# Optimization experiments

Hardware: AMD Instinct MI355X
Metric: run time of the kernel (lower is better)

Reference implementation:

```python
import jax, jax.numpy as jnp
import numpy as np

# Model/config constants
N = 2048          # total nodes in batch
G = 32            # number of graphs
NPG = 64          # nodes per graph (N = G * NPG)
E = 16384         # total edges (E//G per graph, unique within graph)
HIDDEN = 256
N_HEADS = 8
HEAD_DIM = HIDDEN // N_HEADS
EDGE_FEAT = 16
SCALE = HEAD_DIM ** -0.5


def setup_inputs() -> dict:
    key = jax.random.key(0)
    ks = jax.random.split(key, 16)
    nodes = jax.random.normal(ks[0], (N, HIDDEN), dtype=jnp.float32)
    edges = jax.random.normal(ks[1], (E, EDGE_FEAT), dtype=jnp.float32)
    n_node = jnp.full((G,), NPG, dtype=jnp.int32)
    # Unique (sender, receiver) pairs within each graph block
    epg = E // G
    gkeys = jax.random.split(ks[2], G)
    perm = jax.vmap(lambda k: jax.random.permutation(k, NPG * NPG)[:epg])(gkeys)  # [G, epg]
    so = perm // NPG
    ro = perm % NPG
    base = (jnp.arange(G, dtype=jnp.int32) * NPG)[:, None]
    senders = (base + so).reshape(-1).astype(jnp.int32)
    receivers = (base + ro).reshape(-1).astype(jnp.int32)
    init = 0.02
    Wq = jax.random.normal(ks[3], (HIDDEN, HIDDEN), jnp.float32) * init
    Wk = jax.random.normal(ks[4], (HIDDEN, HIDDEN), jnp.float32) * init
    Wv = jax.random.normal(ks[5], (HIDDEN, HIDDEN), jnp.float32) * init
    Wo = jax.random.normal(ks[6], (HIDDEN, HIDDEN), jnp.float32) * init
    We = jax.random.normal(ks[7], (EDGE_FEAT, N_HEADS), jnp.float32) * init
    bq = jnp.zeros((HIDDEN,), jnp.float32)
    bk = jnp.zeros((HIDDEN,), jnp.float32)
    bv = jnp.zeros((HIDDEN,), jnp.float32)
    bo = jnp.zeros((HIDDEN,), jnp.float32)
    be = jnp.zeros((N_HEADS,), jnp.float32)
    return {"nodes": nodes, "edges": edges, "n_node": n_node,
            "senders": senders, "receivers": receivers,
            "Wq": Wq, "bq": bq, "Wk": Wk, "bk": bk, "Wv": Wv, "bv": bv,
            "Wo": Wo, "bo": bo, "We": We, "be": be}


def reference(nodes, edges, n_node, senders, receivers,
              Wq, bq, Wk, bk, Wv, bv, Wo, bo, We, be):
    n_nodes = nodes.shape[0]
    n_graphs = n_node.shape[0]
    q = (nodes @ Wq + bq).reshape(n_nodes, N_HEADS, HEAD_DIM)
    k = (nodes @ Wk + bk).reshape(n_nodes, N_HEADS, HEAD_DIM)
    v = (nodes @ Wv + bv).reshape(n_nodes, N_HEADS, HEAD_DIM)
    scores = jnp.einsum('ihd,jhd->ijh', q, k) * SCALE  # [N, N, H]
    graph_idx = jnp.repeat(jnp.arange(n_graphs), n_node, total_repeat_length=n_nodes)
    same_graph = graph_idx[:, None] == graph_idx[None, :]
    scores = scores + jnp.where(same_graph[:, :, None], 0.0, -1e9)
    # Edge bias scattered into [N, N, H] at (receiver, sender)
    edge_bias = edges @ We + be  # [E, H]
    edge_bias_matrix = jnp.zeros((n_nodes, n_nodes, N_HEADS), dtype=scores.dtype)
    edge_bias_matrix = edge_bias_matrix.at[receivers, senders].set(edge_bias)
    scores = scores + edge_bias_matrix
    attn = jax.nn.softmax(scores, axis=1)  # softmax over key axis j
    out = jnp.einsum('ijh,jhd->ihd', attn, v).reshape(n_nodes, HIDDEN)
    return out @ Wo + bo
```

## Files before the change

### kernel.cpp

```cpp
#include <hip/hip_runtime.h>

#define N_NODES 2048
#define N_GRAPHS 32
#define NPG 64
#define N_EDGES 16384
#define EPG 512
#define HIDDEN 256
#define NHEADS 8
#define HEADDIM 32
#define EDGEFEAT 16
#define ATT_SCALE 0.17677669529663687f

typedef unsigned short u16;
typedef __attribute__((ext_vector_type(8))) short bf16x8;
typedef __attribute__((ext_vector_type(4))) float f32x4;

__device__ __forceinline__ u16 f2b(float f) {
    unsigned x = __float_as_uint(f);
    return (u16)((x + 0x7fffu + ((x >> 16) & 1u)) >> 16);
}
__device__ __forceinline__ unsigned pack2(float a, float b) {
    return (unsigned)f2b(a) | ((unsigned)f2b(b) << 16);
}

__global__ __launch_bounds__(256)
void prep_kernel(const float* __restrict__ Wq, const float* __restrict__ Wk,
                 const float* __restrict__ Wv, const float* __restrict__ Wo,
                 const float* __restrict__ edges, const float* __restrict__ We,
                 const float* __restrict__ be,
                 u16* __restrict__ WT, float* __restrict__ ebias)
{
    const int b = blockIdx.x, tid = threadIdx.x;
    __shared__ float shm[64 * 65];

    if (b < 64) {
        if (tid < EDGEFEAT * NHEADS) shm[tid] = We[tid];
        if (tid < NHEADS) shm[128 + tid] = be[tid];
        __syncthreads();
        const int e = b * 256 + tid;
        const float* ef = edges + (size_t)e * EDGEFEAT;
        float f[EDGEFEAT];
        *(float4*)&f[0]  = *(const float4*)(ef + 0);
        *(float4*)&f[4]  = *(const float4*)(ef + 4);
        *(float4*)&f[8]  = *(const float4*)(ef + 8);
        *(float4*)&f[12] = *(const float4*)(ef + 12);
        float a[NHEADS];
        #pragma unroll
        for (int h = 0; h < NHEADS; ++h) a[h] = shm[128 + h];
        #pragma unroll
        for (int i = 0; i < EDGEFEAT; ++i)
            #pragma unroll
            for (int h = 0; h < NHEADS; ++h) a[h] += f[i] * shm[i * 8 + h];
        float* dst = ebias + (size_t)e * NHEADS;
        *(float4*)(dst)     = make_float4(a[0], a[1], a[2], a[3]);
        *(float4*)(dst + 4) = make_float4(a[4], a[5], a[6], a[7]);
    } else {
        const int bb = b - 64;
        const int m = bb >> 4, t = bb & 15;
        const int k0 = (t >> 2) * 64, n0 = (t & 3) * 64;
        const float* src = (m == 0) ? Wq : (m == 1) ? Wk : (m == 2) ? Wv : Wo;
        #pragma unroll
        for (int rep = 0; rep < 4; ++rep) {
            const int q = rep * 256 + tid;
            const int row = q >> 4, c4 = (q & 15) * 4;
            float4 x = *(const float4*)(src + (size_t)(k0 + row) * HIDDEN + n0 + c4);
            shm[row * 65 + c4 + 0] = x.x;
            shm[row * 65 + c4 + 1] = x.y;
            shm[row * 65 + c4 + 2] = x.z;
            shm[row * 65 + c4 + 3] = x.w;
        }
        __syncthreads();
        u16* dst = WT + (size_t)m * HIDDEN * HIDDEN;
        #pragma unroll
        for (int rep = 0; rep < 2; ++rep) {
            const int nl = (tid >> 3) + rep * 32;
            const int k8 = (tid & 7) * 8;
            uint4 o;
            o.x = pack2(shm[(k8 + 0) * 65 + nl], shm[(k8 + 1) * 65 + nl]);
            o.y = pack2(shm[(k8 + 2) * 65 + nl], shm[(k8 + 3) * 65 + nl]);
            o.z = pack2(shm[(k8 + 4) * 65 + nl], shm[(k8 + 5) * 65 + nl]);
            o.w = pack2(shm[(k8 + 6) * 65 + nl], shm[(k8 + 7) * 65 + nl]);
            *(uint4*)(dst + (size_t)(n0 + nl) * HIDDEN + k0 + k8) = o;
        }
    }
}

__global__ __launch_bounds__(256)
void qkv_attn_kernel(const float* __restrict__ nodes,
                     const u16* __restrict__ WT,
                     const float* __restrict__ bq, const float* __restrict__ bk,
                     const float* __restrict__ bv,
                     const float* __restrict__ ebias,
                     const int* __restrict__ senders,
                     const int* __restrict__ receivers,
                     u16* __restrict__ attnb)
{
    const int g = blockIdx.x, h = blockIdx.y;
    const int tid = threadIdx.x;
    const int lane = tid & 63, wv = tid >> 6;
    const int l16 = lane & 15, quad = lane >> 4;

    __shared__ __align__(16) unsigned char smem[84480];
    short* An = (short*)smem;
    short* Wt = (short*)smem + 64 * 264;
    float* qs = (float*)smem;
    float* ks = qs + 64 * 33;
    float* vs = ks + 64 * 33;
    float* sc = vs + 64 * 33;
    float* red = sc + 64 * 65;

    #pragma unroll
    for (int rep = 0; rep < 16; ++rep) {
        const int q = rep * 256 + tid;
        const int row = q >> 6, f4 = q & 63;
        float4 x = *(const float4*)(nodes + (size_t)(g * NPG + row) * HIDDEN + f4 * 4);
        *(uint2*)&An[row * 264 + f4 * 4] = make_uint2(pack2(x.x, x.y), pack2(x.z, x.w));
    }
    #pragma unroll
    for (int m = 0; m < 3; ++m) {
        const u16* src = WT + (size_t)m * HIDDEN * HIDDEN + (size_t)(h * HEADDIM) * HIDDEN;
        #pragma unroll
        for (int rep = 0; rep < 4; ++rep) {
            const int q = rep * 256 + tid;
            const int row = q >> 5, u = q & 31;
            uint4 x = *(const uint4*)(src + (size_t)row * HIDDEN + u * 8);
            *(uint4*)&Wt[(m * 32 + row) * 264 + u * 8] = x;
        }
    }
    __syncthreads();

    f32x4 acc[6];
    #pragma unroll
    for (int nt = 0; nt < 6; ++nt) acc[nt] = (f32x4){0.f, 0.f, 0.f, 0.f};
    const int arow = (wv * 16 + l16) * 264 + quad * 8;
    #pragma unroll
    for (int k0 = 0; k0 < HIDDEN; k0 += 32) {
        bf16x8 af = *(const bf16x8*)&An[arow + k0];
        #pragma unroll
        for (int nt = 0; nt < 6; ++nt) {
            bf16x8 bf = *(const bf16x8*)&Wt[(nt * 16 + l16) * 264 + k0 + quad * 8];
            acc[nt] = __builtin_amdgcn_mfma_f32_16x16x32_bf16(af, bf, acc[nt], 0, 0, 0);
        }
    }
    __syncthreads();

    #pragma unroll
    for (int nt = 0; nt < 6; ++nt) {
        const int tns = nt >> 1;
        const int col = (nt & 1) * 16 + l16;
        const float* bp = (tns == 0) ? bq : (tns == 1) ? bk : bv;
        const float bias = bp[h * HEADDIM + col];
        float* dst = (tns == 0) ? qs : (tns == 1) ? ks : vs;
        #pragma unroll
        for (int r = 0; r < 4; ++r)
            dst[(wv * 16 + quad * 4 + r) * 33 + col] = acc[nt][r] + bias;
    }
    __syncthreads();

    const int i  = tid & 63;
    const int cg = tid >> 6;

    {
        float qr[HEADDIM];
        #pragma unroll
        for (int d = 0; d < HEADDIM; ++d) qr[d] = qs[i * 33 + d];
        #pragma unroll
        for (int jj = 0; jj < 16; ++jj) {
            const int j = cg * 16 + jj;
            float s = 0.f;
            #pragma unroll
            for (int d = 0; d < HEADDIM; ++d) s += qr[d] * ks[j * 33 + d];
            sc[i * 65 + j] = s * ATT_SCALE;
        }
    }
    __syncthreads();

    {
        #pragma unroll
        for (int rep = 0; rep < 2; ++rep) {
            const int e = g * EPG + rep * 256 + tid;
            const float b = ebias[(size_t)e * NHEADS + h];
            const int s_l = senders[e] & (NPG - 1);
            const int r_l = receivers[e] & (NPG - 1);
            sc[r_l * 65 + s_l] += b;
        }
    }
    __syncthreads();

    {
        float* red_m = red;
        float* red_s = red + 4 * 64;
        float m = -1e30f;
        #pragma unroll
        for (int jj = 0; jj < 16; ++jj) m = fmaxf(m, sc[i * 65 + cg * 16 + jj]);
        red_m[cg * 64 + i] = m;
        __syncthreads();
        m = fmaxf(fmaxf(red_m[0 * 64 + i], red_m[1 * 64 + i]),
                  fmaxf(red_m[2 * 64 + i], red_m[3 * 64 + i]));
        float s = 0.f;
        #pragma unroll
        for (int jj = 0; jj < 16; ++jj) {
            const int j = cg * 16 + jj;
            float e = __expf(sc[i * 65 + j] - m);
            sc[i * 65 + j] = e;
            s += e;
        }
        red_s[cg * 64 + i] = s;
        __syncthreads();
        const float inv = 1.f / (red_s[0 * 64 + i] + red_s[1 * 64 + i] +
                                 red_s[2 * 64 + i] + red_s[3 * 64 + i]);
        #pragma unroll
        for (int jj = 0; jj < 16; ++jj) sc[i * 65 + cg * 16 + jj] *= inv;
    }
    __syncthreads();

    {
        const int row = tid >> 2;
        const int d0 = (tid & 3) * 8;
        float a8[8] = {0, 0, 0, 0, 0, 0, 0, 0};
        for (int j = 0; j < NPG; ++j) {
            const float p = sc[row * 65 + j];
            #pragma unroll
            for (int dd = 0; dd < 8; ++dd) a8[dd] += p * vs[j * 33 + d0 + dd];
        }
        uint4 o;
        o.x = pack2(a8[0], a8[1]);
        o.y = pack2(a8[2], a8[3]);
        o.z = pack2(a8[4], a8[5]);
        o.w = pack2(a8[6], a8[7]);
        *(uint4*)(attnb + (size_t)(g * NPG + row) * HIDDEN + h * HEADDIM + d0) = o;
    }
}

__global__ __launch_bounds__(256)
void outproj_kernel(const u16* __restrict__ A,
                    const u16* __restrict__ BT,
                    const float* __restrict__ bo,
                    float* __restrict__ C)
{
    const int n0 = blockIdx.x * 64, m0 = blockIdx.y * 64;
    const int tid = threadIdx.x;
    const int lane = tid & 63, wv = tid >> 6;
    const int l16 = lane & 15, quad = lane >> 4;

    __shared__ __align__(16) short Ab[64 * 264];
    __shared__ __align__(16) short Bb[64 * 264];

    #pragma unroll
    for (int rep = 0; rep < 8; ++rep) {
        const int q = rep * 256 + tid;
        const int row = q >> 5, u = q & 31;
        *(uint4*)&Ab[row * 264 + u * 8] = *(const uint4*)(A + (size_t)(m0 + row) * HIDDEN + u * 8);
        *(uint4*)&Bb[row * 264 + u * 8] = *(const uint4*)(BT + (size_t)(n0 + row) * HIDDEN + u * 8);
    }
    __syncthreads();

    f32x4 acc[4];
    #pragma unroll
    for (int nt = 0; nt < 4; ++nt) acc[nt] = (f32x4){0.f, 0.f, 0.f, 0.f};
    const int arow = (wv * 16 + l16) * 264 + quad * 8;
    #pragma unroll
    for (int k0 = 0; k0 < HIDDEN; k0 += 32) {
        bf16x8 af = *(const bf16x8*)&Ab[arow + k0];
        #pragma unroll
        for (int nt = 0; nt < 4; ++nt) {
            bf16x8 bf = *(const bf16x8*)&Bb[(nt * 16 + l16) * 264 + k0 + quad * 8];
            acc[nt] = __builtin_amdgcn_mfma_f32_16x16x32_bf16(af, bf, acc[nt], 0, 0, 0);
        }
    }

    #pragma unroll
    for (int nt = 0; nt < 4; ++nt) {
        const int col = n0 + nt * 16 + l16;
        const float bias = bo[col];
        #pragma unroll
        for (int r = 0; r < 4; ++r)
            C[(size_t)(m0 + wv * 16 + quad * 4 + r) * HIDDEN + col] = acc[nt][r] + bias;
    }
}

extern "C" void kernel_launch(void* const* d_in, const int* in_sizes, int n_in,
                              void* d_out, int out_size, void* d_ws, size_t ws_size,
                              hipStream_t stream)
{
    const float* nodes     = (const float*)d_in[0];
    const float* edges     = (const float*)d_in[1];
    const int*   senders   = (const int*)d_in[3];
    const int*   receivers = (const int*)d_in[4];
    const float* Wq = (const float*)d_in[5];
    const float* bq = (const float*)d_in[6];
    const float* Wk = (const float*)d_in[7];
    const float* bk = (const float*)d_in[8];
    const float* Wv = (const float*)d_in[9];
    const float* bv = (const float*)d_in[10];
    const float* Wo = (const float*)d_in[11];
    const float* bo = (const float*)d_in[12];
    const float* We = (const float*)d_in[13];
    const float* be = (const float*)d_in[14];
    float* out = (float*)d_out;

    u16*   WT    = (u16*)d_ws;
    float* ebias = (float*)(WT + (size_t)4 * HIDDEN * HIDDEN);
    u16*   attnb = (u16*)(ebias + (size_t)N_EDGES * NHEADS);
    u16*   WoT   = WT + (size_t)3 * HIDDEN * HIDDEN;

    prep_kernel<<<dim3(128), dim3(256), 0, stream>>>(Wq, Wk, Wv, Wo, edges, We, be,
                                                     WT, ebias);
    qkv_attn_kernel<<<dim3(N_GRAPHS, NHEADS), dim3(256), 0, stream>>>(
        nodes, WT, bq, bk, bv, ebias, senders, receivers, attnb);
    outproj_kernel<<<dim3(HIDDEN / 64, N_NODES / 64), dim3(256), 0, stream>>>(
        attnb, WoT, bo, out);
}
```

Before: 99.47 us.

## Fuse weight prep and edge bias into attention kernels, use MFMA for scores

Drops the separate prep kernel. Weight transpose and bf16 conversion now happen inside the attention and output-projection kernels, and the edge bias is computed per head inline. QK^T and PV are moved from scalar FP32 loops to bf16 MFMA, with a hi/lo split to keep accuracy close to FP32. This removes one launch and a workspace round trip. In exchange, each block redoes the weight conversion, the transposing shared-memory stores are strided and may bank-conflict, and the split-precision approach adds extra MFMAs.

Result: faster. 93.70 us, median of 2 (-5.8%).

```diff
diff --git a/kernel.cpp b/kernel.cpp
--- a/kernel.cpp
+++ b/kernel.cpp
@@ -19,81 +19,23 @@
     unsigned x = __float_as_uint(f);
     return (u16)((x + 0x7fffu + ((x >> 16) & 1u)) >> 16);
 }
+__device__ __forceinline__ float b2f(u16 u) {
+    return __uint_as_float(((unsigned)u) << 16);
+}
 __device__ __forceinline__ unsigned pack2(float a, float b) {
     return (unsigned)f2b(a) | ((unsigned)f2b(b) << 16);
 }
 
 __global__ __launch_bounds__(256)
-void prep_kernel(const float* __restrict__ Wq, const float* __restrict__ Wk,
-                 const float* __restrict__ Wv, const float* __restrict__ Wo,
-                 const float* __restrict__ edges, const float* __restrict__ We,
-                 const float* __restrict__ be,
-                 u16* __restrict__ WT, float* __restrict__ ebias)
-{
-    const int b = blockIdx.x, tid = threadIdx.x;
-    __shared__ float shm[64 * 65];
-
-    if (b < 64) {
-        if (tid < EDGEFEAT * NHEADS) shm[tid] = We[tid];
-        if (tid < NHEADS) shm[128 + tid] = be[tid];
-        __syncthreads();
-        const int e = b * 256 + tid;
-        const float* ef = edges + (size_t)e * EDGEFEAT;
-        float f[EDGEFEAT];
-        *(float4*)&f[0]  = *(const float4*)(ef + 0);
-        *(float4*)&f[4]  = *(const float4*)(ef + 4);
-        *(float4*)&f[8]  = *(const float4*)(ef + 8);
-        *(float4*)&f[12] = *(const float4*)(ef + 12);
-        float a[NHEADS];
-        #pragma unroll
-        for (int h = 0; h < NHEADS; ++h) a[h] = shm[128 + h];
-        #pragma unroll
-        for (int i = 0; i < EDGEFEAT; ++i)
-            #pragma unroll
-            for (int h = 0; h < NHEADS; ++h) a[h] += f[i] * shm[i * 8 + h];
-        float* dst = ebias + (size_t)e * NHEADS;
-        *(float4*)(dst)     = make_float4(a[0], a[1], a[2], a[3]);
-        *(float4*)(dst + 4) = make_float4(a[4], a[5], a[6], a[7]);
-    } else {
-        const int bb = b - 64;
-        const int m = bb >> 4, t = bb & 15;
-        const int k0 = (t >> 2) * 64, n0 = (t & 3) * 64;
-        const float* src = (m == 0) ? Wq : (m == 1) ? Wk : (m == 2) ? Wv : Wo;
-        #pragma unroll
-        for (int rep = 0; rep < 4; ++rep) {
-            const int q = rep * 256 + tid;
-            const int row = q >> 4, c4 = (q & 15) * 4;
-            float4 x = *(const float4*)(src + (size_t)(k0 + row) * HIDDEN + n0 + c4);
-            shm[row * 65 + c4 + 0] = x.x;
-            shm[row * 65 + c4 + 1] = x.y;
-            shm[row * 65 + c4 + 2] = x.z;
-            shm[row * 65 + c4 + 3] = x.w;
-        }
-        __syncthreads();
-        u16* dst = WT + (size_t)m * HIDDEN * HIDDEN;
-        #pragma unroll
-        for (int rep = 0; rep < 2; ++rep) {
-            const int nl = (tid >> 3) + rep * 32;
-            const int k8 = (tid & 7) * 8;
-            uint4 o;
-            o.x = pack2(shm[(k8 + 0) * 65 + nl], shm[(k8 + 1) * 65 + nl]);
-            o.y = pack2(shm[(k8 + 2) * 65 + nl], shm[(k8 + 3) * 65 + nl]);
-            o.z = pack2(shm[(k8 + 4) * 65 + nl], shm[(k8 + 5) * 65 + nl]);
-            o.w = pack2(shm[(k8 + 6) * 65 + nl], shm[(k8 + 7) * 65 + nl]);
-            *(uint4*)(dst + (size_t)(n0 + nl) * HIDDEN + k0 + k8) = o;
-        }
-    }
-}
-
-__global__ __launch_bounds__(256)
-void qkv_attn_kernel(const float* __restrict__ nodes,
-                     const u16* __restrict__ WT,
-                     const float* __restrict__ bq, const float* __restrict__ bk,
-                     const float* __restrict__ bv,
-                     const float* __restrict__ ebias,
-                     const int* __restrict__ senders,
-                     const int* __restrict__ receivers,
-                     u16* __restrict__ attnb)
+void qkv_attn_fused(const float* __restrict__ nodes,
+                    const float* __restrict__ Wq, const float* __restrict__ Wk,
+                    const float* __restrict__ Wv,
+                    const float* __restrict__ bq, const float* __restrict__ bk,
+                    const float* __restrict__ bv,
+                    const float* __restrict__ edges, const float* __restrict__ We,
+                    const float* __restrict__ be,
+                    const int* __restrict__ senders, const int* __restrict__ receivers,
+                    u16* __restrict__ attnb)
 {
     const int g = blockIdx.x, h = blockIdx.y;
     const int tid = threadIdx.x;
@@ -103,11 +45,18 @@
     __shared__ __align__(16) unsigned char smem[84480];
     short* An = (short*)smem;
     short* Wt = (short*)smem + 64 * 264;
-    float* qs = (float*)smem;
-    float* ks = qs + 64 * 33;
-    float* vs = ks + 64 * 33;
-    float* sc = vs + 64 * 33;
+    short* qhi = (short*)smem;
+    short* qlo = qhi + 64 * 40;
+    short* khi = qlo + 64 * 40;
+    short* klo = khi + 64 * 40;
+    short* vsT = klo + 64 * 40;
+    float* sc  = (float*)(smem + 25088);
     float* red = sc + 64 * 65;
+    __shared__ float we_h[EDGEFEAT];
+    __shared__ float sbe;
+
+    if (tid < EDGEFEAT) we_h[tid] = We[tid * NHEADS + h];
+    if (tid == 0) sbe = be[h];
 
     #pragma unroll
     for (int rep = 0; rep < 16; ++rep) {
@@ -117,15 +66,17 @@
         *(uint2*)&An[row * 264 + f4 * 4] = make_uint2(pack2(x.x, x.y), pack2(x.z, x.w));
     }
     #pragma unroll
-    for (int m = 0; m < 3; ++m) {
-        const u16* src = WT + (size_t)m * HIDDEN * HIDDEN + (size_t)(h * HEADDIM) * HIDDEN;
-        #pragma unroll
-        for (int rep = 0; rep < 4; ++rep) {
-            const int q = rep * 256 + tid;
-            const int row = q >> 5, u = q & 31;
-            uint4 x = *(const uint4*)(src + (size_t)row * HIDDEN + u * 8);
-            *(uint4*)&Wt[(m * 32 + row) * 264 + u * 8] = x;
-        }
+    for (int rep = 0; rep < 24; ++rep) {
+        const int q = rep * 256 + tid;
+        const float* Wp = (rep < 8) ? Wq : (rep < 16) ? Wk : Wv;
+        const int r = q & 2047;
+        const int krow = r >> 3, f4 = r & 7;
+        float4 x = *(const float4*)(Wp + (size_t)krow * HIDDEN + h * HEADDIM + f4 * 4);
+        const int nb = (rep >> 3) * 32 + f4 * 4;
+        Wt[(nb + 0) * 264 + krow] = (short)f2b(x.x);
+        Wt[(nb + 1) * 264 + krow] = (short)f2b(x.y);
+        Wt[(nb + 2) * 264 + krow] = (short)f2b(x.z);
+        Wt[(nb + 3) * 264 + krow] = (short)f2b(x.w);
     }
     __syncthreads();
 
@@ -150,44 +101,62 @@
         const int col = (nt & 1) * 16 + l16;
         const float* bp = (tns == 0) ? bq : (tns == 1) ? bk : bv;
         const float bias = bp[h * HEADDIM + col];
-        float* dst = (tns == 0) ? qs : (tns == 1) ? ks : vs;
-        #pragma unroll
-        for (int r = 0; r < 4; ++r)
-            dst[(wv * 16 + quad * 4 + r) * 33 + col] = acc[nt][r] + bias;
-    }
-    __syncthreads();
-
-    const int i  = tid & 63;
-    const int cg = tid >> 6;
+        #pragma unroll
+        for (int r = 0; r < 4; ++r) {
+            const int row = wv * 16 + quad * 4 + r;
+            const float val = acc[nt][r] + bias;
+            if (tns == 2) {
+                vsT[col * 72 + row] = (short)f2b(val);
+            } else {
+                const u16 hi = f2b(val);
+                const u16 lo = f2b(val - b2f(hi));
+                if (tns == 0) { qhi[row * 40 + col] = (short)hi; qlo[row * 40 + col] = (short)lo; }
+                else          { khi[row * 40 + col] = (short)hi; klo[row * 40 + col] = (short)lo; }
+            }
+        }
+    }
+    __syncthreads();
 
     {
-        float qr[HEADDIM];
-        #pragma unroll
-        for (int d = 0; d < HEADDIM; ++d) qr[d] = qs[i * 33 + d];
-        #pragma unroll
-        for (int jj = 0; jj < 16; ++jj) {
-            const int j = cg * 16 + jj;
-            float s = 0.f;
+        bf16x8 qh = *(const bf16x8*)&qhi[(wv * 16 + l16) * 40 + quad * 8];
+        bf16x8 ql = *(const bf16x8*)&qlo[(wv * 16 + l16) * 40 + quad * 8];
+        #pragma unroll
+        for (int nt = 0; nt < 4; ++nt) {
+            bf16x8 kh = *(const bf16x8*)&khi[(nt * 16 + l16) * 40 + quad * 8];
+            bf16x8 kl = *(const bf16x8*)&klo[(nt * 16 + l16) * 40 + quad * 8];
+            f32x4 s = (f32x4){0.f, 0.f, 0.f, 0.f};
+            s = __builtin_amdgcn_mfma_f32_16x16x32_bf16(qh, kh, s, 0, 0, 0);
+            s = __builtin_amdgcn_mfma_f32_16x16x32_bf16(qh, kl, s, 0, 0, 0);
+            s = __builtin_amdgcn_mfma_f32_16x16x32_bf16(ql, kh, s, 0, 0, 0);
             #pragma unroll
-            for (int d = 0; d < HEADDIM; ++d) s += qr[d] * ks[j * 33 + d];
-            sc[i * 65 + j] = s * ATT_SCALE;
-        }
+            for (int r = 0; r < 4; ++r)
+                sc[(wv * 16 + quad * 4 + r) * 65 + nt * 16 + l16] = s[r] * ATT_SCALE;
+        }
+    }
+    __syncthreads();
+
+    #pragma unroll
+    for (int rep = 0; rep < 2; ++rep) {
+        const int e = g * EPG + rep * 256 + tid;
+        const float* ef = edges + (size_t)e * EDGEFEAT;
+        float4 f0 = *(const float4*)(ef + 0);
+        float4 f1 = *(const float4*)(ef + 4);
+        float4 f2 = *(const float4*)(ef + 8);
+        float4 f3 = *(const float4*)(ef + 12);
+        float b = sbe
+            + f0.x * we_h[0]  + f0.y * we_h[1]  + f0.z * we_h[2]  + f0.w * we_h[3]
+            + f1.x * we_h[4]  + f1.y * we_h[5]  + f1.z * we_h[6]  + f1.w * we_h[7]
+            + f2.x * we_h[8]  + f2.y * we_h[9]  + f2.z * we_h[10] + f2.w * we_h[11]
+            + f3.x * we_h[12] + f3.y * we_h[13] + f3.z * we_h[14] + f3.w * we_h[15];
+        const int s_l = senders[e] & (NPG - 1);
+        const int r_l = receivers[e] & (NPG - 1);
+        sc[r_l * 65 + s_l] += b;
     }
     __syncthreads();
 
     {
-        #pragma unroll
-        for (int rep = 0; rep < 2; ++rep) {
-            const int e = g * EPG + rep * 256 + tid;
-            const float b = ebias[(size_t)e * NHEADS + h];
-            const int s_l = senders[e] & (NPG - 1);
-            const int r_l = receivers[e] & (NPG - 1);
-            sc[r_l * 65 + s_l] += b;
-        }
-    }
-    __syncthreads();
-
-    {
+        const int i  = tid & 63;
+        const int cg = tid >> 6;
         float* red_m = red;
         float* red_s = red + 4 * 64;
         float m = -1e30f;
@@ -215,28 +184,53 @@
     __syncthreads();
 
     {
-        const int row = tid >> 2;
-        const int d0 = (tid & 3) * 8;
-        float a8[8] = {0, 0, 0, 0, 0, 0, 0, 0};
-        for (int j = 0; j < NPG; ++j) {
-            const float p = sc[row * 65 + j];
+        f32x4 oacc[2];
+        oacc[0] = (f32x4){0.f, 0.f, 0.f, 0.f};
+        oacc[1] = (f32x4){0.f, 0.f, 0.f, 0.f};
+        #pragma unroll
+        for (int k0 = 0; k0 < NPG; k0 += 32) {
+            float p[8];
             #pragma unroll
-            for (int dd = 0; dd < 8; ++dd) a8[dd] += p * vs[j * 33 + d0 + dd];
-        }
-        uint4 o;
-        o.x = pack2(a8[0], a8[1]);
-        o.y = pack2(a8[2], a8[3]);
-        o.z = pack2(a8[4], a8[5]);
-        o.w = pack2(a8[6], a8[7]);
-        *(uint4*)(attnb + (size_t)(g * NPG + row) * HIDDEN + h * HEADDIM + d0) = o;
+            for (int jj = 0; jj < 8; ++jj)
+                p[jj] = sc[(wv * 16 + l16) * 65 + k0 + quad * 8 + jj];
+            uint4 uh, ul;
+            u16 h0 = f2b(p[0]), h1 = f2b(p[1]), h2 = f2b(p[2]), h3 = f2b(p[3]);
+            u16 h4 = f2b(p[4]), h5 = f2b(p[5]), h6 = f2b(p[6]), h7 = f2b(p[7]);
+            uh.x = (unsigned)h0 | ((unsigned)h1 << 16);
+            uh.y = (unsigned)h2 | ((unsigned)h3 << 16);
+            uh.z = (unsigned)h4 | ((unsigned)h5 << 16);
+            uh.w = (unsigned)h6 | ((unsigned)h7 << 16);
+            ul.x = pack2(p[0] - b2f(h0), p[1] - b2f(h1));
+            ul.y = pack2(p[2] - b2f(h2), p[3] - b2f(h3));
+            ul.z = pack2(p[4] - b2f(h4), p[5] - b2f(h5));
+            ul.w = pack2(p[6] - b2f(h6), p[7] - b2f(h7));
+            bf16x8 ph = *(bf16x8*)&uh;
+            bf16x8 pl = *(bf16x8*)&ul;
+            #pragma unroll
+            for (int nt = 0; nt < 2; ++nt) {
+                bf16x8 vf = *(const bf16x8*)&vsT[(nt * 16 + l16) * 72 + k0 + quad * 8];
+                oacc[nt] = __builtin_amdgcn_mfma_f32_16x16x32_bf16(ph, vf, oacc[nt], 0, 0, 0);
+                oacc[nt] = __builtin_amdgcn_mfma_f32_16x16x32_bf16(pl, vf, oacc[nt], 0, 0, 0);
+            }
+        }
+        #pragma unroll
+        for (int nt = 0; nt < 2; ++nt) {
+            const int d = nt * 16 + l16;
+            #pragma unroll
+            for (int r = 0; r < 4; ++r) {
+                const int row = wv * 16 + quad * 4 + r;
+                attnb[(size_t)(g * NPG + row) * HIDDEN + h * HEADDIM + d] =
+                    f2b(oacc[nt][r]);
+            }
+        }
     }
 }
 
 __global__ __launch_bounds__(256)
-void outproj_kernel(const u16* __restrict__ A,
-                    const u16* __restrict__ BT,
-                    const float* __restrict__ bo,
-                    float* __restrict__ C)
+void outproj_fused(const u16* __restrict__ A,
+                   const float* __restrict__ Wo,
+                   const float* __restrict__ bo,
+                   float* __restrict__ C)
 {
     const int n0 = blockIdx.x * 64, m0 = blockIdx.y * 64;
     const int tid = threadIdx.x;
@@ -250,8 +244,21 @@
     for (int rep = 0; rep < 8; ++rep) {
         const int q = rep * 256 + tid;
         const int row = q >> 5, u = q & 31;
-        *(uint4*)&Ab[row * 264 + u * 8] = *(const uint4*)(A + (size_t)(m0 + row) * HIDDEN + u * 8);
-        *(uint4*)&Bb[row * 264 + u * 8] = *(const uint4*)(BT + (size_t)(n0 + row) * HIDDEN + u * 8);
+        *(uint4*)&Ab[row * 264 + u * 8] =
+            *(const uint4*)(A + (size_t)(m0 + row) * HIDDEN + u * 8);
+    }
+    #pragma unroll
+    for (int rep = 0; rep < 16; ++rep) {
+        const int q = rep * 256 + tid;
+        const int f4 = q & 7;
+        const int krow = (q >> 3) & 255;
+        const int half = q >> 11;
+        float4 x = *(const float4*)(Wo + (size_t)krow * HIDDEN + n0 + half * 32 + f4 * 4);
+        const int nb = half * 32 + f4 * 4;
+        Bb[(nb + 0) * 264 + krow] = (short)f2b(x.x);
+        Bb[(nb + 1) * 264 + krow] = (short)f2b(x.y);
+        Bb[(nb + 2) * 264 + krow] = (short)f2b(x.z);
+        Bb[(nb + 3) * 264 + krow] = (short)f2b(x.w);
     }
     __syncthreads();
 
@@ -299,15 +306,10 @@
     const float* be = (const float*)d_in[14];
     float* out = (float*)d_out;
 
-    u16*   WT    = (u16*)d_ws;
-    float* ebias = (float*)(WT + (size_t)4 * HIDDEN * HIDDEN);
-    u16*   attnb = (u16*)(ebias + (size_t)N_EDGES * NHEADS);
-    u16*   WoT   = WT + (size_t)3 * HIDDEN * HIDDEN;
-
-    prep_kernel<<<dim3(128), dim3(256), 0, stream>>>(Wq, Wk, Wv, Wo, edges, We, be,
-                                                     WT, ebias);
-    qkv_attn_kernel<<<dim3(N_GRAPHS, NHEADS), dim3(256), 0, stream>>>(
-        nodes, WT, bq, bk, bv, ebias, senders, receivers, attnb);
-    outproj_kernel<<<dim3(HIDDEN / 64, N_NODES / 64), dim3(256), 0, stream>>>(
-        attnb, WoT, bo, out);
-}
+    u16* attnb = (u16*)d_ws;
+
+    qkv_attn_fused<<<dim3(N_GRAPHS, NHEADS), dim3(256), 0, stream>>>(
+        nodes, Wq, Wk, Wv, bq, bk, bv, edges, We, be, senders, receivers, attnb);
+    outproj_fused<<<dim3(HIDDEN / 64, N_NODES / 64), dim3(256), 0, stream>>>(
+        attnb, Wo, bo, out);
+}
```
